# Performance work log

Measured on AMD Instinct MI355X. Metric: run time of the kernel, lower is better.

## Reference

```python
import jax, jax.numpy as jnp
import numpy as np

B, T, C = 2, 2048, 2048
H = 16
HD = C // H
MLP_DIM = 4 * C
EPS = 1e-5


def rmsnorm(x):
    return x * jax.lax.rsqrt(jnp.mean(x * x, axis=-1, keepdims=True) + EPS)


def setup_inputs() -> dict:
    key = jax.random.key(0)
    ks = jax.random.split(key, 7)
    s = 0.02
    return {
        "x": jax.random.normal(ks[0], (B, T, C), dtype=jnp.float32),
        "wq": jax.random.normal(ks[1], (C, C), dtype=jnp.float32) * s,
        "wk": jax.random.normal(ks[2], (C, C), dtype=jnp.float32) * s,
        "wv": jax.random.normal(ks[3], (C, C), dtype=jnp.float32) * s,
        "wo": jax.random.normal(ks[4], (C, C), dtype=jnp.float32) * s,
        "fc1": jax.random.normal(ks[5], (MLP_DIM, C), dtype=jnp.float32) * s,
        "fc2": jax.random.normal(ks[6], (C, MLP_DIM), dtype=jnp.float32) * s,
    }


def reference(x, wq, wk, wv, wo, fc1, fc2):
    # --- attention sub-block (pre-norm) ---
    h = rmsnorm(x)
    # nn.Linear applies x @ W.T
    q = (h @ wq.T).reshape(B, T, H, HD).transpose(0, 2, 1, 3)  # [B,H,T,HD]
    k = (h @ wk.T).reshape(B, T, H, HD).transpose(0, 2, 1, 3)
    v = (h @ wv.T).reshape(B, T, H, HD).transpose(0, 2, 1, 3)
    scale = 1.0 / np.sqrt(HD)
    scores = jnp.einsum("bhqd,bhkd->bhqk", q, k) * scale
    causal_mask = jnp.triu(jnp.full((T, T), -jnp.inf, dtype=scores.dtype), k=1)
    scores = scores + causal_mask
    attn = jax.nn.softmax(scores, axis=-1)
    out = jnp.einsum("bhqk,bhkd->bhqd", attn, v)
    out = out.transpose(0, 2, 1, 3).reshape(B, T, C)
    x = x + out @ wo.T
    # --- MLP sub-block (squared ReLU) ---
    h = rmsnorm(x)
    m = h @ fc1.T
    m = jnp.square(jax.nn.relu(m))
    x = x + m @ fc2.T
    return x
```

## Files before the change

### kernel.cpp

```cpp
#include <hip/hip_runtime.h>


typedef __bf16 bf16x8 __attribute__((ext_vector_type(8)));
typedef __bf16 bf16x4 __attribute__((ext_vector_type(4)));
typedef float  f32x4  __attribute__((ext_vector_type(4)));

static __device__ __forceinline__ __bf16 tobf(float f) { return (__bf16)f; }

static __device__ __forceinline__ void async_copy16(const void* g, void* l) {
    __builtin_amdgcn_global_load_lds(
        (const __attribute__((address_space(1))) void*)g,
        (__attribute__((address_space(3))) void*)l, 16, 0, 0);
}

__global__ void detect_dtype_kernel(const unsigned short* __restrict__ xh,
                                    int* __restrict__ flag) {
    int t = threadIdx.x;
    unsigned short u = xh[2 * t];
    int e = (u >> 7) & 0xFF;
    bool outlier = (e < 100) || (e > 131);
    unsigned long long m = __ballot(outlier);
    if (t == 0) *flag = (__popcll(m) >= 16) ? 1 : 0;
}

__global__ __launch_bounds__(256) void convert_w4(
    const void* __restrict__ w0, const void* __restrict__ w1,
    const void* __restrict__ w2, const void* __restrict__ w3,
    __bf16* __restrict__ dqkvo, const int* __restrict__ flagp) {
    constexpr size_t CC = (size_t)2048 * 2048;
    const int y = blockIdx.y;
    size_t i = ((size_t)blockIdx.x * 256 + threadIdx.x) * 8;
    const void* s = (y == 0) ? w0 : (y == 1) ? w1 : (y == 2) ? w2 : w3;
    __bf16* d = dqkvo + (size_t)y * CC;
    if (*flagp != 0) {
        const float4* sp = (const float4*)((const float*)s + i);
        float4 a = sp[0], b = sp[1];
        bf16x8 o = {tobf(a.x), tobf(a.y), tobf(a.z), tobf(a.w),
                    tobf(b.x), tobf(b.y), tobf(b.z), tobf(b.w)};
        *(bf16x8*)(d + i) = o;
    } else {
        *(bf16x8*)(d + i) = *(const bf16x8*)((const __bf16*)s + i);
    }
}

__global__ __launch_bounds__(256) void convert_w1(
    const void* __restrict__ src, __bf16* __restrict__ dst,
    const int* __restrict__ flagp) {
    size_t i = ((size_t)blockIdx.x * 256 + threadIdx.x) * 8;
    if (*flagp != 0) {
        const float4* sp = (const float4*)((const float*)src + i);
        float4 a = sp[0], b = sp[1];
        bf16x8 o = {tobf(a.x), tobf(a.y), tobf(a.z), tobf(a.w),
                    tobf(b.x), tobf(b.y), tobf(b.z), tobf(b.w)};
        *(bf16x8*)(dst + i) = o;
    } else {
        *(bf16x8*)(dst + i) = *(const bf16x8*)((const __bf16*)src + i);
    }
}

template <int SRC>
__global__ __launch_bounds__(256) void rmsnorm_kernel(
    const void* __restrict__ xp, __bf16* __restrict__ h,
    const int* __restrict__ flagp) {
    constexpr int C = 2048;
    const int row = blockIdx.x, t = threadIdx.x;
    float vals[8];
    bool f32in = (SRC == 1) || (*flagp != 0);
    if (f32in) {
        const float4* xr = (const float4*)((const float*)xp + (size_t)row * C);
        float4 a = xr[2 * t], b = xr[2 * t + 1];
        vals[0] = a.x; vals[1] = a.y; vals[2] = a.z; vals[3] = a.w;
        vals[4] = b.x; vals[5] = b.y; vals[6] = b.z; vals[7] = b.w;
    } else {
        bf16x8 a = *((const bf16x8*)((const __bf16*)xp + (size_t)row * C) + t);
#pragma unroll
        for (int j = 0; j < 8; ++j) vals[j] = (float)a[j];
    }
    float ss = 0.f;
#pragma unroll
    for (int j = 0; j < 8; ++j) ss += vals[j] * vals[j];
#pragma unroll
    for (int off = 32; off > 0; off >>= 1) ss += __shfl_down(ss, off);
    __shared__ float red[4];
    if ((t & 63) == 0) red[t >> 6] = ss;
    __syncthreads();
    float mean = (red[0] + red[1] + red[2] + red[3]) * (1.0f / C);
    float sc = rsqrtf(mean + 1e-5f);
    bf16x8 o;
#pragma unroll
    for (int j = 0; j < 8; ++j) o[j] = tobf(vals[j] * sc);
    *((bf16x8*)(h + (size_t)row * C) + t) = o;
}

static __device__ __forceinline__ void gemm_core_128(
    const __bf16* __restrict__ A, const __bf16* __restrict__ W,
    int m0, int n0, int K,
    __bf16 (*As)[64], __bf16 (*Bs)[64], f32x4 (&acc)[4][4]) {
    const int t = threadIdx.x;
    const int wave = t >> 6, lane = t & 63;
    const int lr = lane & 15, lq = lane >> 4;
    const int wm = wave & 1, wn = wave >> 1;

    const __bf16* gA[4];
    const __bf16* gB[4];
    int lo[4];
#pragma unroll
    for (int i = 0; i < 4; ++i) {
        int c = i * 256 + t;
        int row = c >> 3;
        int sl = (c & 7) ^ (row & 7);
        gA[i] = A + (size_t)(m0 + row) * K + sl * 8;
        gB[i] = W + (size_t)(n0 + row) * K + sl * 8;
        lo[i] = (c & ~63) * 8;
    }
    const int sx = lr & 7;

    const f32x4 zero = {0.f, 0.f, 0.f, 0.f};
#pragma unroll
    for (int i = 0; i < 4; ++i)
#pragma unroll
        for (int j = 0; j < 4; ++j) acc[i][j] = zero;

    for (int k0 = 0; k0 < K; k0 += 64) {
#pragma unroll
        for (int i = 0; i < 4; ++i) {
            async_copy16(gA[i] + k0, &As[0][0] + lo[i]);
            async_copy16(gB[i] + k0, &Bs[0][0] + lo[i]);
        }
        __syncthreads();
#pragma unroll
        for (int kk = 0; kk < 2; ++kk) {
            const int sp = ((kk * 4 + lq) ^ sx) * 8;
            bf16x8 a[4], b[4];
#pragma unroll
            for (int ii = 0; ii < 4; ++ii) {
                a[ii] = *(const bf16x8*)&As[wm * 64 + ii * 16 + lr][sp];
                b[ii] = *(const bf16x8*)&Bs[wn * 64 + ii * 16 + lr][sp];
            }
#pragma unroll
            for (int ii = 0; ii < 4; ++ii)
#pragma unroll
                for (int jj = 0; jj < 4; ++jj)
                    acc[ii][jj] = __builtin_amdgcn_mfma_f32_16x16x32_bf16(
                        a[ii], b[jj], acc[ii][jj], 0, 0, 0);
        }
        __syncthreads();
    }
}

template <int EPI>
__global__ __launch_bounds__(256) void gemm_nt(
    const __bf16* __restrict__ A, const __bf16* __restrict__ W,
    void* __restrict__ outp, const void* __restrict__ resp,
    int M, int N, int K, const int* __restrict__ flagp) {
    __shared__ __align__(16) __bf16 As[128][64];
    __shared__ __align__(16) __bf16 Bs[128][64];
    const int t = threadIdx.x;
    const int wave = t >> 6, lane = t & 63;
    const int lr = lane & 15, lq = lane >> 4;
    const int wm = wave & 1, wn = wave >> 1;
    const int m0 = blockIdx.y * 128, n0 = blockIdx.x * 128;

    f32x4 acc[4][4];
    gemm_core_128(A, W, m0, n0, K, As, Bs, acc);

    const bool f32 = (EPI == 2) ? false : (*flagp != 0);
#pragma unroll
    for (int i = 0; i < 4; ++i)
#pragma unroll
        for (int j = 0; j < 4; ++j)
#pragma unroll
            for (int r = 0; r < 4; ++r) {
                int row = m0 + wm * 64 + i * 16 + lq * 4 + r;
                int col = n0 + wn * 64 + j * 16 + lr;
                size_t off = (size_t)row * N + col;
                float v = acc[i][j][r];
                if (EPI == 2) {
                    float rv = v > 0.f ? v : 0.f;
                    ((__bf16*)outp)[off] = tobf(rv * rv);
                } else if (EPI == 5) {
                    float res = f32 ? ((const float*)resp)[off]
                                    : (float)((const __bf16*)resp)[off];
                    ((float*)outp)[off] = v + res;
                } else {
                    float o = v + ((const float*)resp)[off];
                    if (f32) ((float*)outp)[off] = o;
                    else     ((__bf16*)outp)[off] = tobf(o);
                }
            }
}

__global__ __launch_bounds__(256) void gemm_qkv(
    const __bf16* __restrict__ A, const __bf16* __restrict__ Wall,
    __bf16* __restrict__ qout, __bf16* __restrict__ kout,
    __bf16* __restrict__ vtout) {
    constexpr int N = 2048, K = 2048;
    constexpr float kQScale = 1.4426950408889634f * 0.08838834764831845f;
    __shared__ __align__(16) __bf16 As[128][64];
    __shared__ __align__(16) __bf16 Bs[128][64];
    const int t = threadIdx.x;
    const int wave = t >> 6, lane = t & 63;
    const int lr = lane & 15, lq = lane >> 4;
    const int wm = wave & 1, wn = wave >> 1;
    const int which = blockIdx.x >> 4;
    const int m0 = blockIdx.y * 128, n0 = (blockIdx.x & 15) * 128;
    const __bf16* W = Wall + (size_t)which * N * K;

    f32x4 acc[4][4];
    gemm_core_128(A, W, m0, n0, K, As, Bs, acc);

    if (which < 2) {
        __bf16* outp = (which == 0) ? qout : kout;
        const float sc = (which == 0) ? kQScale : 1.0f;
#pragma unroll
        for (int i = 0; i < 4; ++i)
#pragma unroll
            for (int j = 0; j < 4; ++j)
#pragma unroll
                for (int r = 0; r < 4; ++r) {
                    int row = m0 + wm * 64 + i * 16 + lq * 4 + r;
                    int col = n0 + wn * 64 + j * 16 + lr;
                    outp[(size_t)row * N + col] = tobf(acc[i][j][r] * sc);
                }
    } else {
#pragma unroll
        for (int i = 0; i < 4; ++i)
#pragma unroll
            for (int j = 0; j < 4; ++j) {
                int t0 = m0 + wm * 64 + i * 16 + lq * 4;
                int b  = t0 >> 11, tt = t0 & 2047;
                int col = n0 + wn * 64 + j * 16 + lr;
                bf16x4 p = {tobf(acc[i][j][0]), tobf(acc[i][j][1]),
                            tobf(acc[i][j][2]), tobf(acc[i][j][3])};
                *(bf16x4*)(vtout + (((size_t)(b * 2048 + col)) << 11) + tt) = p;
            }
    }
}

__global__ __launch_bounds__(256) void attn_kernel(
    const __bf16* __restrict__ Q, const __bf16* __restrict__ K,
    const __bf16* __restrict__ Vt, __bf16* __restrict__ O) {
    constexpr int T = 2048, C = 2048, HD = 128;
    __shared__ __align__(16) __bf16 Ks[64][136];
    __shared__ __align__(16) __bf16 Vts[128][72];
    __shared__ __align__(16) __bf16 Ps[4][16][72];
    const int t = threadIdx.x, w = t >> 6, lane = t & 63;
    const int lr = lane & 15, lq = lane >> 4;
    const int b = blockIdx.z, h = blockIdx.y;
    const __bf16* vtb = Vt + ((size_t)(b * 2048 + h * 128) << 11);
    const f32x4 zero = {0.f, 0.f, 0.f, 0.f};

    bf16x8 ones;
#pragma unroll
    for (int j = 0; j < 8; ++j) ones[j] = (lr == 0) ? (__bf16)1.0f : (__bf16)0.0f;

    for (int pass = 0; pass < 2; ++pass) {
        const int qblk = (pass == 0) ? blockIdx.x : 31 - blockIdx.x;
        const int q0 = qblk * 64;

        const int qrow = q0 + w * 16 + lr;
        const __bf16* qb = Q + (size_t)(b * T + qrow) * C + h * HD;
        bf16x8 qf[4];
#pragma unroll
        for (int s = 0; s < 4; ++s)
            qf[s] = *(const bf16x8*)(qb + s * 32 + lq * 8);

        f32x4 oacc[8], lacc = zero;
#pragma unroll
        for (int nc = 0; nc < 8; ++nc) oacc[nc] = zero;
        float m_i[4] = {-3e38f, -3e38f, -3e38f, -3e38f};

        for (int kb = 0; kb <= qblk; ++kb) {
            const int k00 = kb * 64;
#pragma unroll
            for (int i = 0; i < 4; ++i) {
                int c = t + 256 * i;
                int r = c >> 4, col = (c & 15) * 8;
                *(bf16x8*)&Ks[r][col] =
                    *(const bf16x8*)(K + (size_t)(b * T + k00 + r) * C + h * HD + col);
            }
#pragma unroll
            for (int i = 0; i < 4; ++i) {
                int c = t + 256 * i;
                int r = c >> 3, cg = (c & 7) * 8;
                *(bf16x8*)&Vts[r][cg] =
                    *(const bf16x8*)(vtb + ((size_t)r << 11) + k00 + cg);
            }
            __syncthreads();

            float pv[4][4];
#pragma unroll
            for (int jc = 0; jc < 4; ++jc) {
                f32x4 s = zero;
#pragma unroll
                for (int ks = 0; ks < 4; ++ks) {
                    bf16x8 kf = *(const bf16x8*)&Ks[jc * 16 + lr][ks * 32 + lq * 8];
                    s = __builtin_amdgcn_mfma_f32_16x16x32_bf16(qf[ks], kf, s, 0, 0, 0);
                }
#pragma unroll
                for (int r = 0; r < 4; ++r) pv[jc][r] = s[r];
            }
            if (kb == qblk) {
#pragma unroll
                for (int jc = 0; jc < 4; ++jc)
#pragma unroll
                    for (int r = 0; r < 4; ++r)
                        if (jc * 16 + lr > w * 16 + lq * 4 + r) pv[jc][r] = -3e38f;
            }
            float rmax[4];
#pragma unroll
            for (int r = 0; r < 4; ++r)
                rmax[r] = fmaxf(fmaxf(pv[0][r], pv[1][r]), fmaxf(pv[2][r], pv[3][r]));
#pragma unroll
            for (int off = 1; off < 16; off <<= 1)
#pragma unroll
                for (int r = 0; r < 4; ++r)
                    rmax[r] = fmaxf(rmax[r], __shfl_xor(rmax[r], off));
            float alpha[4];
#pragma unroll
            for (int r = 0; r < 4; ++r) {
                float mn = fmaxf(m_i[r], rmax[r]);
                alpha[r] = exp2f(m_i[r] - mn);
                m_i[r] = mn;
            }
#pragma unroll
            for (int jc = 0; jc < 4; ++jc)
#pragma unroll
                for (int r = 0; r < 4; ++r)
                    Ps[w][lq * 4 + r][jc * 16 + lr] = tobf(exp2f(pv[jc][r] - m_i[r]));
#pragma unroll
            for (int nc = 0; nc < 8; ++nc)
#pragma unroll
                for (int r = 0; r < 4; ++r) oacc[nc][r] *= alpha[r];
#pragma unroll
            for (int r = 0; r < 4; ++r) lacc[r] *= alpha[r];
            __syncthreads();

#pragma unroll
            for (int s2 = 0; s2 < 2; ++s2) {
                bf16x8 pa = *(const bf16x8*)&Ps[w][lr][s2 * 32 + lq * 8];
#pragma unroll
                for (int nc = 0; nc < 8; ++nc) {
                    bf16x8 vf = *(const bf16x8*)&Vts[nc * 16 + lr][s2 * 32 + lq * 8];
                    oacc[nc] = __builtin_amdgcn_mfma_f32_16x16x32_bf16(
                        pa, vf, oacc[nc], 0, 0, 0);
                }
                lacc = __builtin_amdgcn_mfma_f32_16x16x32_bf16(pa, ones, lacc, 0, 0, 0);
            }
            __syncthreads();
        }

        float inv[4];
#pragma unroll
        for (int r = 0; r < 4; ++r) inv[r] = 1.0f / __shfl(lacc[r], lane & 48);
#pragma unroll
        for (int nc = 0; nc < 8; ++nc)
#pragma unroll
            for (int r = 0; r < 4; ++r) {
                int row = q0 + w * 16 + lq * 4 + r;
                O[(size_t)(b * T + row) * C + h * HD + nc * 16 + lr] =
                    tobf(oacc[nc][r] * inv[r]);
            }
        __syncthreads();
    }
}

extern "C" void kernel_launch(void* const* d_in, const int* in_sizes, int n_in,
                              void* d_out, int out_size, void* d_ws, size_t ws_size,
                              hipStream_t stream) {
    const void* x   = d_in[0];
    const void* wq  = d_in[1];
    const void* wk  = d_in[2];
    const void* wv  = d_in[3];
    const void* wo  = d_in[4];
    const void* fc1 = d_in[5];
    const void* fc2 = d_in[6];
    constexpr int Bv = 2, Tv = 2048, Cv = 2048, Hv = 16, MLP = 8192;
    constexpr int M = Bv * Tv;
    constexpr size_t NE = (size_t)M * Cv;
    constexpr size_t CC = (size_t)Cv * Cv;

    char* ws = (char*)d_ws;
    int*    flag = (int*)ws;
    __bf16* h    = (__bf16*)(ws + 256);
    __bf16* qb   = h  + NE;
    __bf16* kb   = qb + NE;
    __bf16* vt   = kb + NE;
    __bf16* ao   = vt + NE;
    float*  x1   = (float*)(ao + NE);
    __bf16* mm   = (__bf16*)(x1 + NE);
    __bf16* wqkvob = mm;
    __bf16* fc1b   = qb;
    __bf16* fc2b   = vt;

    detect_dtype_kernel<<<1, 64, 0, stream>>>((const unsigned short*)x, flag);

    convert_w4<<<dim3(2048, 4), 256, 0, stream>>>(wq, wk, wv, wo, wqkvob, flag);

    rmsnorm_kernel<0><<<M, 256, 0, stream>>>(x, h, flag);

    gemm_qkv<<<dim3(48, 32), 256, 0, stream>>>(h, wqkvob, qb, kb, vt);

    attn_kernel<<<dim3(16, Hv, Bv), 256, 0, stream>>>(qb, kb, vt, ao);

    convert_w1<<<8192, 256, 0, stream>>>(fc1, fc1b, flag);

    gemm_nt<5><<<dim3(16, 32), 256, 0, stream>>>(ao, wqkvob + 3 * CC, x1, x,
                                                 M, Cv, Cv, flag);

    convert_w1<<<8192, 256, 0, stream>>>(fc2, fc2b, flag);

    rmsnorm_kernel<1><<<M, 256, 0, stream>>>(x1, h, flag);

    gemm_nt<2><<<dim3(64, 32), 256, 0, stream>>>(h, fc1b, mm, nullptr,
                                                 M, MLP, Cv, flag);

    gemm_nt<6><<<dim3(16, 32), 256, 0, stream>>>(mm, fc2b, d_out, x1,
                                                 M, Cv, MLP, flag);
}
```

Baseline: 817.5 us.

## Use 256x256 double-buffered 8-wave GEMM for QKV and MLP projections

Adds a 256x256-tile GEMM core with 512 threads, double-buffered LDS filled by async global-to-LDS copies, barrier-separated phases with raised MFMA priority, and explicit waitcnt fences. The QKV, fc1 and fc2 GEMMs move to this kernel to get more reuse per loaded tile and to overlap loads with compute. The output projection stays on the 128 tile. The large tiles mean fewer blocks (128 for fc2, 384 for QKV, 512 for fc1) on a 256-CU device, which risks poor load balance on the smaller grids, and the 128 KB of LDS per block limits occupancy.

After: 886.9 us. 8.5% more time.

```diff
diff --git a/kernel.cpp b/kernel.cpp
--- a/kernel.cpp
+++ b/kernel.cpp
@@ -12,6 +12,13 @@
         (const __attribute__((address_space(1))) void*)g,
         (__attribute__((address_space(3))) void*)l, 16, 0, 0);
 }
+
+#define LGKM0_FENCE() do { \
+    asm volatile("s_waitcnt lgkmcnt(0)" ::: "memory"); \
+    __builtin_amdgcn_sched_barrier(0); } while (0)
+#define VMCNT8_FENCE() do { \
+    asm volatile("s_waitcnt vmcnt(8)" ::: "memory"); \
+    __builtin_amdgcn_sched_barrier(0); } while (0)
 
 __global__ void detect_dtype_kernel(const unsigned short* __restrict__ xh,
                                     int* __restrict__ flag) {
@@ -92,6 +99,234 @@
     *((bf16x8*)(h + (size_t)row * C) + t) = o;
 }
 
+static __device__ __forceinline__ void gemm_core_256(
+    const __bf16* __restrict__ A, const __bf16* __restrict__ W,
+    int m0, int n0, int K,
+    __bf16 (*As)[256][64], __bf16 (*Bs)[256][64], f32x4 (&acc)[8][4]) {
+    const int tid = threadIdx.x;
+    const int wave = tid >> 6, lane = tid & 63;
+    const int lr = lane & 15, lq = lane >> 4;
+    const int wm = wave >> 2, wn = wave & 3;
+    const int sx = lr & 7;
+    const int NT = K >> 6;
+
+    int off[4], lo[4];
+#pragma unroll
+    for (int i = 0; i < 4; ++i) {
+        int c = i * 512 + tid;
+        int row = c >> 3;
+        off[i] = row * K + (((c & 7) ^ (row & 7)) * 8);
+        lo[i] = (c & ~63) * 8;
+    }
+
+    const f32x4 zero = {0.f, 0.f, 0.f, 0.f};
+#pragma unroll
+    for (int m = 0; m < 8; ++m)
+#pragma unroll
+        for (int n = 0; n < 4; ++n) acc[m][n] = zero;
+
+#pragma unroll
+    for (int pt = 0; pt < 2; ++pt) {
+        const __bf16* ga = A + (size_t)m0 * K + pt * 64;
+        const __bf16* gb = W + (size_t)n0 * K + pt * 64;
+#pragma unroll
+        for (int i = 0; i < 4; ++i)
+            async_copy16(ga + off[i], &As[pt][0][0] + lo[i]);
+#pragma unroll
+        for (int i = 0; i < 4; ++i)
+            async_copy16(gb + off[i], &Bs[pt][0][0] + lo[i]);
+    }
+    VMCNT8_FENCE();
+    __builtin_amdgcn_s_barrier();
+
+    for (int t = 0; t < NT; ++t) {
+        const int bi = t & 1;
+        const __bf16 (*Ac)[64] = As[bi];
+        const __bf16 (*Bc)[64] = Bs[bi];
+        const int ts = (t + 2 < NT) ? t + 2 : NT - 1;
+        const __bf16* gAt = A + (size_t)m0 * K + (size_t)ts * 64;
+        const __bf16* gBt = W + (size_t)n0 * K + (size_t)ts * 64;
+
+        bf16x8 a0[4][2], a1[4][2], b0[2][2], b1[2][2];
+
+#pragma unroll
+        for (int m = 0; m < 4; ++m)
+#pragma unroll
+            for (int kk = 0; kk < 2; ++kk)
+                a0[m][kk] = *(const bf16x8*)
+                    &Ac[wm * 128 + m * 16 + lr][((kk * 4 + lq) ^ sx) * 8];
+#pragma unroll
+        for (int n = 0; n < 2; ++n)
+#pragma unroll
+            for (int kk = 0; kk < 2; ++kk)
+                b0[n][kk] = *(const bf16x8*)
+                    &Bc[wn * 64 + n * 16 + lr][((kk * 4 + lq) ^ sx) * 8];
+        __builtin_amdgcn_s_barrier();
+        LGKM0_FENCE();
+        __builtin_amdgcn_s_setprio(1);
+#pragma unroll
+        for (int m = 0; m < 4; ++m)
+#pragma unroll
+            for (int n = 0; n < 2; ++n)
+#pragma unroll
+                for (int kk = 0; kk < 2; ++kk)
+                    acc[m][n] = __builtin_amdgcn_mfma_f32_16x16x32_bf16(
+                        a0[m][kk], b0[n][kk], acc[m][n], 0, 0, 0);
+        __builtin_amdgcn_s_setprio(0);
+        __builtin_amdgcn_s_barrier();
+
+#pragma unroll
+        for (int m = 0; m < 4; ++m)
+#pragma unroll
+            for (int kk = 0; kk < 2; ++kk)
+                a1[m][kk] = *(const bf16x8*)
+                    &Ac[wm * 128 + (m + 4) * 16 + lr][((kk * 4 + lq) ^ sx) * 8];
+        __builtin_amdgcn_s_barrier();
+        LGKM0_FENCE();
+        __builtin_amdgcn_s_setprio(1);
+#pragma unroll
+        for (int m = 0; m < 4; ++m)
+#pragma unroll
+            for (int n = 0; n < 2; ++n)
+#pragma unroll
+                for (int kk = 0; kk < 2; ++kk)
+                    acc[m + 4][n] = __builtin_amdgcn_mfma_f32_16x16x32_bf16(
+                        a1[m][kk], b0[n][kk], acc[m + 4][n], 0, 0, 0);
+        __builtin_amdgcn_s_setprio(0);
+        __builtin_amdgcn_s_barrier();
+
+#pragma unroll
+        for (int n = 0; n < 2; ++n)
+#pragma unroll
+            for (int kk = 0; kk < 2; ++kk)
+                b1[n][kk] = *(const bf16x8*)
+                    &Bc[wn * 64 + (n + 2) * 16 + lr][((kk * 4 + lq) ^ sx) * 8];
+#pragma unroll
+        for (int i = 0; i < 4; ++i)
+            async_copy16(gAt + off[i], &As[bi][0][0] + lo[i]);
+        __builtin_amdgcn_s_barrier();
+        LGKM0_FENCE();
+        __builtin_amdgcn_s_setprio(1);
+#pragma unroll
+        for (int m = 0; m < 4; ++m)
+#pragma unroll
+            for (int n = 0; n < 2; ++n)
+#pragma unroll
+                for (int kk = 0; kk < 2; ++kk)
+                    acc[m + 4][n + 2] = __builtin_amdgcn_mfma_f32_16x16x32_bf16(
+                        a1[m][kk], b1[n][kk], acc[m + 4][n + 2], 0, 0, 0);
+        __builtin_amdgcn_s_setprio(0);
+        __builtin_amdgcn_s_barrier();
+
+#pragma unroll
+        for (int i = 0; i < 4; ++i)
+            async_copy16(gBt + off[i], &Bs[bi][0][0] + lo[i]);
+        __builtin_amdgcn_s_barrier();
+        LGKM0_FENCE();
+        __builtin_amdgcn_s_setprio(1);
+#pragma unroll
+        for (int m = 0; m < 4; ++m)
+#pragma unroll
+            for (int n = 0; n < 2; ++n)
+#pragma unroll
+                for (int kk = 0; kk < 2; ++kk)
+                    acc[m][n + 2] = __builtin_amdgcn_mfma_f32_16x16x32_bf16(
+                        a0[m][kk], b1[n][kk], acc[m][n + 2], 0, 0, 0);
+        __builtin_amdgcn_s_setprio(0);
+        VMCNT8_FENCE();
+        __builtin_amdgcn_s_barrier();
+    }
+}
+
+template <int EPI>
+__global__ __launch_bounds__(512, 2) void gemm256_nt(
+    const __bf16* __restrict__ A, const __bf16* __restrict__ W,
+    void* __restrict__ outp, const void* __restrict__ resp,
+    int M, int N, int K, const int* __restrict__ flagp) {
+    __shared__ __align__(16) __bf16 As[2][256][64];
+    __shared__ __align__(16) __bf16 Bs[2][256][64];
+    const int tid = threadIdx.x;
+    const int wave = tid >> 6, lane = tid & 63;
+    const int lr = lane & 15, lq = lane >> 4;
+    const int wm = wave >> 2, wn = wave & 3;
+    const int m0 = blockIdx.y * 256, n0 = blockIdx.x * 256;
+
+    f32x4 acc[8][4];
+    gemm_core_256(A, W, m0, n0, K, As, Bs, acc);
+
+    const bool f32 = (EPI == 2) ? false : (*flagp != 0);
+#pragma unroll
+    for (int m = 0; m < 8; ++m)
+#pragma unroll
+        for (int n = 0; n < 4; ++n)
+#pragma unroll
+            for (int r = 0; r < 4; ++r) {
+                int row = m0 + wm * 128 + m * 16 + lq * 4 + r;
+                int col = n0 + wn * 64 + n * 16 + lr;
+                size_t o = (size_t)row * N + col;
+                float v = acc[m][n][r];
+                if (EPI == 2) {
+                    float rv = v > 0.f ? v : 0.f;
+                    ((__bf16*)outp)[o] = tobf(rv * rv);
+                } else if (EPI == 5) {
+                    float res = f32 ? ((const float*)resp)[o]
+                                    : (float)((const __bf16*)resp)[o];
+                    ((float*)outp)[o] = v + res;
+                } else {
+                    float ov = v + ((const float*)resp)[o];
+                    if (f32) ((float*)outp)[o] = ov;
+                    else     ((__bf16*)outp)[o] = tobf(ov);
+                }
+            }
+}
+
+__global__ __launch_bounds__(512, 2) void gemm256_qkv(
+    const __bf16* __restrict__ A, const __bf16* __restrict__ Wall,
+    __bf16* __restrict__ qout, __bf16* __restrict__ kout,
+    __bf16* __restrict__ vtout) {
+    constexpr int N = 2048, K = 2048;
+    constexpr float kQScale = 1.4426950408889634f * 0.08838834764831845f;
+    __shared__ __align__(16) __bf16 As[2][256][64];
+    __shared__ __align__(16) __bf16 Bs[2][256][64];
+    const int tid = threadIdx.x;
+    const int wave = tid >> 6, lane = tid & 63;
+    const int lr = lane & 15, lq = lane >> 4;
+    const int wm = wave >> 2, wn = wave & 3;
+    const int which = blockIdx.x >> 3;
+    const int m0 = blockIdx.y * 256, n0 = (blockIdx.x & 7) * 256;
+    const __bf16* W = Wall + (size_t)which * N * K;
+
+    f32x4 acc[8][4];
+    gemm_core_256(A, W, m0, n0, K, As, Bs, acc);
+
+    if (which < 2) {
+        __bf16* outp = (which == 0) ? qout : kout;
+        const float sc = (which == 0) ? kQScale : 1.0f;
+#pragma unroll
+        for (int m = 0; m < 8; ++m)
+#pragma unroll
+            for (int n = 0; n < 4; ++n)
+#pragma unroll
+                for (int r = 0; r < 4; ++r) {
+                    int row = m0 + wm * 128 + m * 16 + lq * 4 + r;
+                    int col = n0 + wn * 64 + n * 16 + lr;
+                    outp[(size_t)row * N + col] = tobf(acc[m][n][r] * sc);
+                }
+    } else {
+#pragma unroll
+        for (int m = 0; m < 8; ++m)
+#pragma unroll
+            for (int n = 0; n < 4; ++n) {
+                int t0 = m0 + wm * 128 + m * 16 + lq * 4;
+                int b  = t0 >> 11, tt = t0 & 2047;
+                int col = n0 + wn * 64 + n * 16 + lr;
+                bf16x4 p = {tobf(acc[m][n][0]), tobf(acc[m][n][1]),
+                            tobf(acc[m][n][2]), tobf(acc[m][n][3])};
+                *(bf16x4*)(vtout + (((size_t)(b * 2048 + col)) << 11) + tt) = p;
+            }
+    }
+}
+
 static __device__ __forceinline__ void gemm_core_128(
     const __bf16* __restrict__ A, const __bf16* __restrict__ W,
     int m0, int n0, int K,
@@ -148,10 +383,9 @@
     }
 }
 
-template <int EPI>
-__global__ __launch_bounds__(256) void gemm_nt(
+__global__ __launch_bounds__(256) void gemm128_wo(
     const __bf16* __restrict__ A, const __bf16* __restrict__ W,
-    void* __restrict__ outp, const void* __restrict__ resp,
+    float* __restrict__ outp, const void* __restrict__ resp,
     int M, int N, int K, const int* __restrict__ flagp) {
     __shared__ __align__(16) __bf16 As[128][64];
     __shared__ __align__(16) __bf16 Bs[128][64];
@@ -164,7 +398,7 @@
     f32x4 acc[4][4];
     gemm_core_128(A, W, m0, n0, K, As, Bs, acc);
 
-    const bool f32 = (EPI == 2) ? false : (*flagp != 0);
+    const bool f32 = (*flagp != 0);
 #pragma unroll
     for (int i = 0; i < 4; ++i)
 #pragma unroll
@@ -173,68 +407,11 @@
             for (int r = 0; r < 4; ++r) {
                 int row = m0 + wm * 64 + i * 16 + lq * 4 + r;
                 int col = n0 + wn * 64 + j * 16 + lr;
-                size_t off = (size_t)row * N + col;
-                float v = acc[i][j][r];
-                if (EPI == 2) {
-                    float rv = v > 0.f ? v : 0.f;
-                    ((__bf16*)outp)[off] = tobf(rv * rv);
-                } else if (EPI == 5) {
-                    float res = f32 ? ((const float*)resp)[off]
-                                    : (float)((const __bf16*)resp)[off];
-                    ((float*)outp)[off] = v + res;
-                } else {
-                    float o = v + ((const float*)resp)[off];
-                    if (f32) ((float*)outp)[off] = o;
-                    else     ((__bf16*)outp)[off] = tobf(o);
-                }
-            }
-}
-
-__global__ __launch_bounds__(256) void gemm_qkv(
-    const __bf16* __restrict__ A, const __bf16* __restrict__ Wall,
-    __bf16* __restrict__ qout, __bf16* __restrict__ kout,
-    __bf16* __restrict__ vtout) {
-    constexpr int N = 2048, K = 2048;
-    constexpr float kQScale = 1.4426950408889634f * 0.08838834764831845f;
-    __shared__ __align__(16) __bf16 As[128][64];
-    __shared__ __align__(16) __bf16 Bs[128][64];
-    const int t = threadIdx.x;
-    const int wave = t >> 6, lane = t & 63;
-    const int lr = lane & 15, lq = lane >> 4;
-    const int wm = wave & 1, wn = wave >> 1;
-    const int which = blockIdx.x >> 4;
-    const int m0 = blockIdx.y * 128, n0 = (blockIdx.x & 15) * 128;
-    const __bf16* W = Wall + (size_t)which * N * K;
-
-    f32x4 acc[4][4];
-    gemm_core_128(A, W, m0, n0, K, As, Bs, acc);
-
-    if (which < 2) {
-        __bf16* outp = (which == 0) ? qout : kout;
-        const float sc = (which == 0) ? kQScale : 1.0f;
-#pragma unroll
-        for (int i = 0; i < 4; ++i)
-#pragma unroll
-            for (int j = 0; j < 4; ++j)
-#pragma unroll
-                for (int r = 0; r < 4; ++r) {
-                    int row = m0 + wm * 64 + i * 16 + lq * 4 + r;
-                    int col = n0 + wn * 64 + j * 16 + lr;
-                    outp[(size_t)row * N + col] = tobf(acc[i][j][r] * sc);
-                }
-    } else {
-#pragma unroll
-        for (int i = 0; i < 4; ++i)
-#pragma unroll
-            for (int j = 0; j < 4; ++j) {
-                int t0 = m0 + wm * 64 + i * 16 + lq * 4;
-                int b  = t0 >> 11, tt = t0 & 2047;
-                int col = n0 + wn * 64 + j * 16 + lr;
-                bf16x4 p = {tobf(acc[i][j][0]), tobf(acc[i][j][1]),
-                            tobf(acc[i][j][2]), tobf(acc[i][j][3])};
-                *(bf16x4*)(vtout + (((size_t)(b * 2048 + col)) << 11) + tt) = p;
-            }
-    }
+                size_t o = (size_t)row * N + col;
+                float res = f32 ? ((const float*)resp)[o]
+                                : (float)((const __bf16*)resp)[o];
+                outp[o] = acc[i][j][r] + res;
+            }
 }
 
 __global__ __launch_bounds__(256) void attn_kernel(
@@ -399,22 +576,22 @@
 
     rmsnorm_kernel<0><<<M, 256, 0, stream>>>(x, h, flag);
 
-    gemm_qkv<<<dim3(48, 32), 256, 0, stream>>>(h, wqkvob, qb, kb, vt);
+    gemm256_qkv<<<dim3(24, 16), 512, 0, stream>>>(h, wqkvob, qb, kb, vt);
 
     attn_kernel<<<dim3(16, Hv, Bv), 256, 0, stream>>>(qb, kb, vt, ao);
 
     convert_w1<<<8192, 256, 0, stream>>>(fc1, fc1b, flag);
 
-    gemm_nt<5><<<dim3(16, 32), 256, 0, stream>>>(ao, wqkvob + 3 * CC, x1, x,
+    gemm128_wo<<<dim3(16, 32), 256, 0, stream>>>(ao, wqkvob + 3 * CC, x1, x,
                                                  M, Cv, Cv, flag);
 
     convert_w1<<<8192, 256, 0, stream>>>(fc2, fc2b, flag);
 
     rmsnorm_kernel<1><<<M, 256, 0, stream>>>(x1, h, flag);
 
-    gemm_nt<2><<<dim3(64, 32), 256, 0, stream>>>(h, fc1b, mm, nullptr,
-                                                 M, MLP, Cv, flag);
-
-    gemm_nt<6><<<dim3(16, 32), 256, 0, stream>>>(mm, fc2b, d_out, x1,
-                                                 M, Cv, MLP, flag);
-}
+    gemm256_nt<2><<<dim3(32, 16), 512, 0, stream>>>(h, fc1b, mm, nullptr,
+                                                    M, MLP, Cv, flag);
+
+    gemm256_nt<6><<<dim3(8, 16), 512, 0, stream>>>(mm, fc2b, d_out, x1,
+                                                   M, Cv, MLP, flag);
+}
```
